# Kernel tuning notes

Hardware: AMD Instinct MI355X
Metric: run time of the kernel (lower is better)

The kernel has to match this reference:

```python
import jax, jax.numpy as jnp
from jax import lax
import numpy as np

KSIZE = 3        # patch-matching kernel
RATE = 2         # dilation/upsample rate
FUSE_K = 3       # fusion kernel size
SCALE = 10.0     # softmax scale
EPS = 1e-4


def _same_pads(size, k, s):
    # TF 'SAME' padding: total pad so out = ceil(size / s)
    out = -(-size // s)
    total = max(0, (out - 1) * s + k - size)
    top = total // 2
    return (top, total - top)


def _extract_patches(x, k, s):
    # x: [N,C,H,W] -> [N, L, C, k, k], SAME padding, row-major patch order
    ph = _same_pads(x.shape[2], k, s)
    pw = _same_pads(x.shape[3], k, s)
    p = lax.conv_general_dilated_patches(x, (k, k), (s, s), (ph, pw))
    N, _, Ho, Wo = p.shape
    C = x.shape[1]
    p = p.reshape(N, C, k, k, Ho * Wo)  # channel-major patch layout (matches torch unfold)
    return jnp.transpose(p, (0, 4, 1, 2, 3))


def setup_inputs() -> dict:
    key = jax.random.key(0)
    k1, k2 = jax.random.split(key)
    f = jax.random.normal(k1, (8, 96, 64, 64), dtype=jnp.float32)
    b = jax.random.normal(k2, (8, 96, 64, 64), dtype=jnp.float32)
    return {"f": f, "b": b}


def reference(f, b):
    # TF-style nearest-neighbor downsample (stride sampling)
    fs = f[:, :, ::RATE, ::RATE]
    bs = b[:, :, ::RATE, ::RATE]
    N, C, H, W = fs.shape  # downsampled dims; f and b share shape here
    L = H * W
    kernel = 2 * RATE

    # raw background patches for aggregation: [N, L, C, 2r, 2r]
    raw_w = _extract_patches(b, kernel, RATE)
    # matching patches from downsampled background: [N, L, C, 3, 3]
    w = _extract_patches(bs, KSIZE, 1)

    fuse_w = jnp.eye(FUSE_K, dtype=f.dtype).reshape(1, 1, FUSE_K, FUSE_K)
    ct_pad = kernel - 1 - 1  # conv_transpose padding=1 -> conv pad k-1-p = 2

    def attend(xi, wi, rwi):
        # xi: [C,H,W]; wi: [L,C,3,3]; rwi: [L,C,2r,2r]
        norm = jnp.sqrt(jnp.sum(wi * wi, axis=(1, 2, 3), keepdims=True))
        wn = wi / jnp.maximum(norm, EPS)
        # cosine-similarity correlation: [L,H,W]
        yi = lax.conv_general_dilated(xi[None], wn, (1, 1), ((1, 1), (1, 1)))[0]
        # fusion: identity-kernel convs over the [L_b, L_f] score map, both orientations
        y2 = yi.reshape(1, 1, L, L)
        y2 = lax.conv_general_dilated(y2, fuse_w, (1, 1), ((1, 1), (1, 1)))
        y2 = jnp.transpose(y2.reshape(H, W, H, W), (1, 0, 3, 2)).reshape(1, 1, L, L)
        y2 = lax.conv_general_dilated(y2, fuse_w, (1, 1), ((1, 1), (1, 1)))
        yi = jnp.transpose(y2.reshape(W, H, W, H), (1, 0, 3, 2)).reshape(L, H, W)
        # softmax over background patches (mask mm == 1 since mask is None)
        yi = jax.nn.softmax(yi * SCALE, axis=0)
        # conv_transpose2d(yi, rwi, stride=RATE, padding=1) / 4
        wct = jnp.flip(jnp.swapaxes(rwi, 0, 1), axis=(2, 3))  # [C, L, 2r, 2r]
        out = lax.conv_general_dilated(
            yi[None], wct, (1, 1), ((ct_pad, ct_pad), (ct_pad, ct_pad)),
            lhs_dilation=(RATE, RATE))[0]
        return out / 4.0

    y = jax.vmap(attend)(fs, w, raw_w)  # [N, C, H*RATE, W*RATE]
    return y.reshape(f.shape)
```

## Files before the change

kernel.cpp:

```cpp
#include <hip/hip_runtime.h>
#include <math.h>

#define NB 8
#define NC 96
#define HF 64
#define HS 32
#define L 1024
#define MN 1536

#define G_OFF    0ull
#define F1T_OFF  (8ull * 1024 * 1024)
#define YB_B     (64ull * 1024 * 1024)
#define RWT_B    (80ull * 1024 * 1024)
#define N_OFF    (27262976ull)
#define FS_OFF   (27271168ull)
#define BS_OFF   (28057600ull)
#define Z_OFF    0ull

typedef __attribute__((ext_vector_type(8))) short short8;
typedef __attribute__((ext_vector_type(4))) float float4v;

__device__ inline unsigned short f2bf(float x) {
    union { float f; unsigned u; } v; v.f = x;
    unsigned r = v.u + 0x7fff + ((v.u >> 16) & 1);
    return (unsigned short)(r >> 16);
}

__global__ void kprep(const float* __restrict__ f, const float* __restrict__ b,
                      float* __restrict__ ws) {
    int n = blockIdx.x, c = blockIdx.y, z = blockIdx.z;
    int t = threadIdx.x;
    if (z == 0) {
        const float* src = f + ((size_t)n * NC + c) * (HF * HF);
        float* dst = ws + FS_OFF + ((size_t)n * NC + c) * 1024;
        #pragma unroll
        for (int e = 0; e < 4; ++e) {
            int pos = t + e * 256;
            int i = pos >> 5, j = pos & 31;
            dst[pos] = src[(2 * i) * HF + 2 * j];
        }
        return;
    }
    __shared__ float pl[64][65];
    const float* bp = b + ((size_t)n * NC + c) * (HF * HF);
    for (int e = 0; e < 16; ++e) {
        int idx = t + e * 256;
        pl[idx >> 6][idx & 63] = bp[idx];
    }
    __syncthreads();
    float* bs = ws + BS_OFF + ((size_t)n * NC + c) * 1024;
    #pragma unroll
    for (int e = 0; e < 4; ++e) {
        int pos = t + e * 256;
        int i = pos >> 5, j = pos & 31;
        bs[pos] = pl[2 * i][2 * j];
    }
    unsigned short* RWtF = (unsigned short*)((char*)ws + RWT_B) + (size_t)n * MN * L
                           + (size_t)c * 32 * 512;
    #pragma unroll
    for (int uv = 0; uv < 16; ++uv) {
        int u = uv >> 2, v = uv & 3;
        for (int e = 0; e < 4; ++e) {
            int k = t + e * 256;
            int ly = k & 31, lx = k >> 5;
            int r = 2 * ly - 1 + u, s = 2 * lx - 1 + v;
            float val = (r >= 0 && r < HF && s >= 0 && s < HF) ? pl[r][s] : 0.f;
            int kc = k >> 5, qd = (k >> 3) & 3, j = k & 7;
            RWtF[(size_t)kc * 512 + (qd * 16 + uv) * 8 + j] = f2bf(val);
        }
    }
}

__global__ void k0_norm(float* __restrict__ ws) {
    int n = blockIdx.x;
    int t = threadIdx.x;
    int i = t >> 5, j = t & 31;
    __shared__ float sq[1024];
    const float* bsp = ws + BS_OFF + (size_t)n * NC * 1024;
    float s = 0.f;
    for (int c = 0; c < NC; ++c) {
        float v = bsp[(size_t)c * 1024 + t];
        s += v * v;
    }
    sq[t] = s;
    __syncthreads();
    float nsq = 0.f;
    #pragma unroll
    for (int dy = -1; dy <= 1; ++dy)
        #pragma unroll
        for (int dx = -1; dx <= 1; ++dx) {
            int ii = i + dy, jj = j + dx;
            if (ii >= 0 && ii < HS && jj >= 0 && jj < HS) nsq += sq[ii * HS + jj];
        }
    ws[N_OFF + (size_t)n * L + t] = 1.f / fmaxf(sqrtf(nsq), 1e-4f);
}

__global__ __launch_bounds__(256) void k1_gram(float* __restrict__ ws) {
    int n = blockIdx.x;
    int p0 = blockIdx.y * 128, l0 = blockIdx.z * 128;
    int t = threadIdx.x;
    int tp = t >> 4, tm = t & 15;
    __shared__ float Bt[32][132];
    __shared__ float Ft[32][132];
    float acc[8][8] = {};
    const float* bsp = ws + BS_OFF + (size_t)n * NC * 1024;
    const float* fsp = ws + FS_OFF + (size_t)n * NC * 1024;
    for (int c0 = 0; c0 < NC; c0 += 32) {
        #pragma unroll
        for (int e = 0; e < 4; ++e) {
            int idx = t + e * 256;
            int cl = idx >> 5, vq = idx & 31;
            *(float4*)&Bt[cl][vq * 4] =
                *(const float4*)&bsp[(size_t)(c0 + cl) * 1024 + l0 + vq * 4];
            *(float4*)&Ft[cl][vq * 4] =
                *(const float4*)&fsp[(size_t)(c0 + cl) * 1024 + p0 + vq * 4];
        }
        __syncthreads();
        for (int cl = 0; cl < 32; ++cl) {
            float4 a0 = *(const float4*)&Bt[cl][tp * 8];
            float4 a1 = *(const float4*)&Bt[cl][tp * 8 + 4];
            float4 b0 = *(const float4*)&Ft[cl][tm * 8];
            float4 b1 = *(const float4*)&Ft[cl][tm * 8 + 4];
            float av[8] = {a0.x, a0.y, a0.z, a0.w, a1.x, a1.y, a1.z, a1.w};
            float bv[8] = {b0.x, b0.y, b0.z, b0.w, b1.x, b1.y, b1.z, b1.w};
            #pragma unroll
            for (int aa = 0; aa < 8; ++aa)
                #pragma unroll
                for (int bb = 0; bb < 8; ++bb)
                    acc[aa][bb] += av[aa] * bv[bb];
        }
        __syncthreads();
    }
    float* G = ws + G_OFF + (size_t)n * L * L;
    #pragma unroll
    for (int aa = 0; aa < 8; ++aa) {
        int l = l0 + tp * 8 + aa;
        *(float4*)&G[(size_t)l * L + p0 + tm * 8] =
            make_float4(acc[aa][0], acc[aa][1], acc[aa][2], acc[aa][3]);
        *(float4*)&G[(size_t)l * L + p0 + tm * 8 + 4] =
            make_float4(acc[aa][4], acc[aa][5], acc[aa][6], acc[aa][7]);
    }
}

__global__ __launch_bounds__(256) void k23_score_fuse1t(float* __restrict__ ws) {
    int bid = blockIdx.x;
    int n = bid & 7;
    int tile = bid >> 3;
    int i0 = (tile >> 5) * 32, j0 = (tile & 31) * 32;
    int t = threadIdx.x;
    __shared__ float U[36][37];
    __shared__ float sA[34][35];
    __shared__ float sinv[34];
    const float* G = ws + G_OFF + (size_t)n * L * L;
    const float* invn = ws + N_OFF + (size_t)n * L;
    if (t < 34) {
        int l = i0 - 1 + t;
        sinv[t] = ((unsigned)l < L) ? invn[l] : 0.f;
    }
    for (int e = 0; e < 6; ++e) {
        int idx = t + e * 256;
        if (idx < 1296) {
            int a = idx / 36, bq = idx - a * 36;
            int l = i0 - 2 + a, p = j0 - 2 + bq;
            float s = 0.f;
            #pragma unroll
            for (int dy = -1; dy <= 1; ++dy) {
                int ll = l + dy * 32, pp = p + dy * 32;
                if ((unsigned)ll < L && (unsigned)pp < L)
                    s += G[(size_t)ll * L + pp];
            }
            U[a][bq] = s;
        }
    }
    __syncthreads();
    for (int e = 0; e < 5; ++e) {
        int idx = t + e * 256;
        if (idx < 1156) {
            int ih = idx / 34, jh = idx - ih * 34;
            int l = i0 - 1 + ih, p = j0 - 1 + jh;
            float a = 0.f;
            if ((unsigned)l < L && (unsigned)p < L) {
                int lx = l & 31, px = p & 31;
                float s = 0.f;
                #pragma unroll
                for (int dx = -1; dx <= 1; ++dx) {
                    bool ok = (unsigned)(lx + dx) < HS && (unsigned)(px + dx) < HS;
                    float u = U[ih + 1 + dx][jh + 1 + dx];
                    s += ok ? u : 0.f;
                }
                a = sinv[ih] * s;
            }
            sA[ih][jh] = a;
        }
    }
    __syncthreads();
    float* F1T = ws + F1T_OFF + (size_t)n * L * L;
    #pragma unroll
    for (int e = 0; e < 4; ++e) {
        int idx = t + e * 256;
        int jl = idx >> 5, il = idx & 31;
        float v = sA[il][jl] + sA[il + 1][jl + 1] + sA[il + 2][jl + 2];
        F1T[(size_t)(j0 + jl) * L + i0 + il] = v;
    }
}

__global__ __launch_bounds__(256) void k4_fuse2_softmax(float* __restrict__ ws) {
    int n = blockIdx.x, px = blockIdx.y, py0 = blockIdx.z * 4;
    int t = threadIdx.x;
    __shared__ float trow[6][32][33];
    const float* F1T = ws + F1T_OFF + (size_t)n * L * L;
    int Jbase = px * HS + py0;
    #pragma unroll
    for (int e = 0; e < 6; ++e) {
        int idx = t + e * 256;
        int d = idx >> 8, q = idx & 255;
        int Jd = Jbase + d - 1;
        float4 v = make_float4(0.f, 0.f, 0.f, 0.f);
        if ((unsigned)Jd < L) {
            int rd = (Jd & 31) * HS + (Jd >> 5);
            v = *(const float4*)&F1T[(size_t)rd * L + 4 * q];
        }
        int col = q >> 3, r0 = (4 * q) & 31;
        trow[d][r0 + 0][col] = v.x;
        trow[d][r0 + 1][col] = v.y;
        trow[d][r0 + 2][col] = v.z;
        trow[d][r0 + 3][col] = v.w;
    }
    __syncthreads();
    int w = t >> 6, ln = t & 63;
    int py = py0 + w;
    int p = py * HS + px;
    float vals[16];
    float mymax = -1e30f;
    #pragma unroll
    for (int e = 0; e < 16; ++e) {
        int k = e * 64 + ln;
        float v = 0.f;
        #pragma unroll
        for (int d = 0; d < 3; ++d) {
            int kd = k + d - 1;
            if ((unsigned)kd < L) v += trow[w + d][kd >> 5][kd & 31];
        }
        v *= 10.0f;
        vals[e] = v;
        mymax = fmaxf(mymax, v);
    }
    #pragma unroll
    for (int off = 32; off > 0; off >>= 1)
        mymax = fmaxf(mymax, __shfl_xor(mymax, off));
    float mysum = 0.f;
    #pragma unroll
    for (int e = 0; e < 16; ++e) { vals[e] = __expf(vals[e] - mymax); mysum += vals[e]; }
    #pragma unroll
    for (int off = 32; off > 0; off >>= 1)
        mysum += __shfl_xor(mysum, off);
    float rinv = 1.f / mysum;
    unsigned short* YbF = (unsigned short*)((char*)ws + YB_B) + (size_t)n * L * L;
    int pt = p >> 4, fr = p & 15;
    #pragma unroll
    for (int e = 0; e < 16; ++e) {
        int k = e * 64 + ln;
        int kc = k >> 5, qd = (k >> 3) & 3, j = k & 7;
        YbF[((size_t)pt * 32 + kc) * 512 + (qd * 16 + fr) * 8 + j] = f2bf(vals[e] * rinv);
    }
}

__global__ __launch_bounds__(256) void k6_mfma_z(float* __restrict__ ws) {
    int n = blockIdx.x;
    int wv = threadIdx.x >> 6, lane = threadIdx.x & 63;
    int pt0 = blockIdx.z * 8 + (wv >> 1) * 4;
    int mt0 = blockIdx.y * 8 + (wv & 1) * 4;

    const unsigned short* YbF = (const unsigned short*)((const char*)ws + YB_B)
                                + (size_t)n * L * L + lane * 8;
    const unsigned short* RWtF = (const unsigned short*)((const char*)ws + RWT_B)
                                 + (size_t)n * MN * L + lane * 8;

    float4v acc[4][4] = {};
    short8 af[2][4], bf[2][4];
    #pragma unroll
    for (int a = 0; a < 4; ++a) {
        af[0][a] = *(const short8*)(YbF + ((size_t)(pt0 + a) * 32) * 512);
        bf[0][a] = *(const short8*)(RWtF + ((size_t)(mt0 + a) * 32) * 512);
    }
    for (int kc = 0; kc < 32; ++kc) {
        int cur = kc & 1, nxt = cur ^ 1;
        if (kc < 31) {
            #pragma unroll
            for (int a = 0; a < 4; ++a) {
                af[nxt][a] = *(const short8*)(YbF + ((size_t)(pt0 + a) * 32 + kc + 1) * 512);
                bf[nxt][a] = *(const short8*)(RWtF + ((size_t)(mt0 + a) * 32 + kc + 1) * 512);
            }
        }
        #pragma unroll
        for (int a = 0; a < 4; ++a)
            #pragma unroll
            for (int bq = 0; bq < 4; ++bq)
                acc[a][bq] = __builtin_amdgcn_mfma_f32_16x16x32_bf16(
                    af[cur][a], bf[cur][bq], acc[a][bq], 0, 0, 0);
    }

    int fr = lane & 15, qd = lane >> 4;
    float* Zp = ws + Z_OFF + (size_t)n * L * MN;
    #pragma unroll
    for (int a = 0; a < 4; ++a) {
        #pragma unroll
        for (int r = 0; r < 4; ++r) {
            int p = (pt0 + a) * 16 + qd * 4 + r;
            #pragma unroll
            for (int bq = 0; bq < 4; ++bq) {
                int m = (mt0 + bq) * 16 + fr;
                Zp[(size_t)p * MN + m] = acc[a][bq][r];
            }
        }
    }
}

__global__ __launch_bounds__(256) void k7_gather(const float* __restrict__ ws,
                                                 float* __restrict__ out) {
    int n = blockIdx.x, yq = blockIdx.y, c = blockIdx.z;
    int t = threadIdx.x;
    int y0 = yq * 4;
    int ibase = (y0 >> 1) - 1;
    __shared__ float zs[128][17];
    const float* Zp = ws + Z_OFF + (size_t)n * L * MN;
    #pragma unroll
    for (int e = 0; e < 2; ++e) {
        int idx = t + e * 256;
        int pl = idx >> 2, q = idx & 3;
        int il = pl >> 5, j = pl & 31;
        int i = ibase + il;
        float4 v = make_float4(0.f, 0.f, 0.f, 0.f);
        if (i >= 0 && i < HS)
            v = *(const float4*)&Zp[(size_t)(i * HS + j) * MN + c * 16 + q * 4];
        zs[pl][q * 4 + 0] = v.x;
        zs[pl][q * 4 + 1] = v.y;
        zs[pl][q * 4 + 2] = v.z;
        zs[pl][q * 4 + 3] = v.w;
    }
    __syncthreads();
    int y = y0 + (t >> 6), x = t & 63;
    int ih = (y + 1) >> 1, jh = (x + 1) >> 1;
    float s = 0.f;
    #pragma unroll
    for (int di = 0; di < 2; ++di) {
        int i = ih - di;
        if (i < 0 || i >= HS) continue;
        int u = y + 1 - 2 * i;
        int il = i - ibase;
        #pragma unroll
        for (int dj = 0; dj < 2; ++dj) {
            int j = jh - dj;
            if (j < 0 || j >= HS) continue;
            int v = x + 1 - 2 * j;
            s += zs[il * 32 + j][u * 4 + v];
        }
    }
    out[(((size_t)n * NC + c) * HF + y) * HF + x] = 0.25f * s;
}

extern "C" void kernel_launch(void* const* d_in, const int* in_sizes, int n_in,
                              void* d_out, int out_size, void* d_ws, size_t ws_size,
                              hipStream_t stream) {
    const float* f = (const float*)d_in[0];
    const float* b = (const float*)d_in[1];
    float* out = (float*)d_out;
    float* ws = (float*)d_ws;

    kprep<<<dim3(NB, NC, 2), 256, 0, stream>>>(f, b, ws);
    k0_norm<<<NB, 1024, 0, stream>>>(ws);
    k1_gram<<<dim3(NB, 8, 8), 256, 0, stream>>>(ws);
    k23_score_fuse1t<<<8192, 256, 0, stream>>>(ws);
    k4_fuse2_softmax<<<dim3(NB, 32, 8), 256, 0, stream>>>(ws);
    k6_mfma_z<<<dim3(NB, 12, 8), 256, 0, stream>>>(ws);
    k7_gather<<<dim3(NB, 16, 96), 256, 0, stream>>>(ws, out);
}
```

Baseline: 200.7 us.

## Vectorize RWt packing stores, retile MFMA Z GEMM, gather two channels per block

```diff
diff --git a/kernel.cpp b/kernel.cpp
--- a/kernel.cpp
+++ b/kernel.cpp
@@ -57,17 +57,23 @@
     }
     unsigned short* RWtF = (unsigned short*)((char*)ws + RWT_B) + (size_t)n * MN * L
                            + (size_t)c * 32 * 512;
-    #pragma unroll
-    for (int uv = 0; uv < 16; ++uv) {
-        int u = uv >> 2, v = uv & 3;
-        for (int e = 0; e < 4; ++e) {
-            int k = t + e * 256;
-            int ly = k & 31, lx = k >> 5;
-            int r = 2 * ly - 1 + u, s = 2 * lx - 1 + v;
-            float val = (r >= 0 && r < HF && s >= 0 && s < HF) ? pl[r][s] : 0.f;
-            int kc = k >> 5, qd = (k >> 3) & 3, j = k & 7;
-            RWtF[(size_t)kc * 512 + (qd * 16 + uv) * 8 + j] = f2bf(val);
-        }
+    int wv = t >> 6, ln = t & 63;
+    int qd = ln >> 4, uv = ln & 15;
+    int u = uv >> 2, v = uv & 3;
+    #pragma unroll
+    for (int it = 0; it < 8; ++it) {
+        int kc = it * 4 + wv;
+        short8 out8;
+        int s = 2 * kc - 1 + v;
+        bool sok = (s >= 0 && s < HF);
+        #pragma unroll
+        for (int j = 0; j < 8; ++j) {
+            int ly = qd * 8 + j;
+            int r = 2 * ly - 1 + u;
+            float val = (sok && r >= 0 && r < HF) ? pl[r][s] : 0.f;
+            out8[j] = (short)f2bf(val);
+        }
+        *(short8*)(RWtF + (size_t)kc * 512 + ln * 8) = out8;
     }
 }
 
@@ -269,33 +275,35 @@
     int n = blockIdx.x;
     int wv = threadIdx.x >> 6, lane = threadIdx.x & 63;
     int pt0 = blockIdx.z * 8 + (wv >> 1) * 4;
-    int mt0 = blockIdx.y * 8 + (wv & 1) * 4;
+    int mt0 = blockIdx.y * 6 + (wv & 1) * 3;
 
     const unsigned short* YbF = (const unsigned short*)((const char*)ws + YB_B)
                                 + (size_t)n * L * L + lane * 8;
     const unsigned short* RWtF = (const unsigned short*)((const char*)ws + RWT_B)
                                  + (size_t)n * MN * L + lane * 8;
 
-    float4v acc[4][4] = {};
-    short8 af[2][4], bf[2][4];
-    #pragma unroll
-    for (int a = 0; a < 4; ++a) {
+    float4v acc[4][3] = {};
+    short8 af[2][4], bf[2][3];
+    #pragma unroll
+    for (int a = 0; a < 4; ++a)
         af[0][a] = *(const short8*)(YbF + ((size_t)(pt0 + a) * 32) * 512);
-        bf[0][a] = *(const short8*)(RWtF + ((size_t)(mt0 + a) * 32) * 512);
-    }
+    #pragma unroll
+    for (int bq = 0; bq < 3; ++bq)
+        bf[0][bq] = *(const short8*)(RWtF + ((size_t)(mt0 + bq) * 32) * 512);
     for (int kc = 0; kc < 32; ++kc) {
         int cur = kc & 1, nxt = cur ^ 1;
         if (kc < 31) {
             #pragma unroll
-            for (int a = 0; a < 4; ++a) {
+            for (int a = 0; a < 4; ++a)
                 af[nxt][a] = *(const short8*)(YbF + ((size_t)(pt0 + a) * 32 + kc + 1) * 512);
-                bf[nxt][a] = *(const short8*)(RWtF + ((size_t)(mt0 + a) * 32 + kc + 1) * 512);
-            }
+            #pragma unroll
+            for (int bq = 0; bq < 3; ++bq)
+                bf[nxt][bq] = *(const short8*)(RWtF + ((size_t)(mt0 + bq) * 32 + kc + 1) * 512);
         }
         #pragma unroll
         for (int a = 0; a < 4; ++a)
             #pragma unroll
-            for (int bq = 0; bq < 4; ++bq)
+            for (int bq = 0; bq < 3; ++bq)
                 acc[a][bq] = __builtin_amdgcn_mfma_f32_16x16x32_bf16(
                     af[cur][a], bf[cur][bq], acc[a][bq], 0, 0, 0);
     }
@@ -308,7 +316,7 @@
         for (int r = 0; r < 4; ++r) {
             int p = (pt0 + a) * 16 + qd * 4 + r;
             #pragma unroll
-            for (int bq = 0; bq < 4; ++bq) {
+            for (int bq = 0; bq < 3; ++bq) {
                 int m = (mt0 + bq) * 16 + fr;
                 Zp[(size_t)p * MN + m] = acc[a][bq][r];
             }
@@ -318,21 +326,21 @@
 
 __global__ __launch_bounds__(256) void k7_gather(const float* __restrict__ ws,
                                                  float* __restrict__ out) {
-    int n = blockIdx.x, yq = blockIdx.y, c = blockIdx.z;
+    int n = blockIdx.x, yq = blockIdx.y, c0 = blockIdx.z * 2;
     int t = threadIdx.x;
     int y0 = yq * 4;
     int ibase = (y0 >> 1) - 1;
-    __shared__ float zs[128][17];
+    __shared__ float zs[128][33];
     const float* Zp = ws + Z_OFF + (size_t)n * L * MN;
     #pragma unroll
-    for (int e = 0; e < 2; ++e) {
-        int idx = t + e * 256;
-        int pl = idx >> 2, q = idx & 3;
+    for (int e = 0; e < 4; ++e) {
+        int idx = t + e * 256;
+        int pl = idx >> 3, q = idx & 7;
         int il = pl >> 5, j = pl & 31;
         int i = ibase + il;
         float4 v = make_float4(0.f, 0.f, 0.f, 0.f);
         if (i >= 0 && i < HS)
-            v = *(const float4*)&Zp[(size_t)(i * HS + j) * MN + c * 16 + q * 4];
+            v = *(const float4*)&Zp[(size_t)(i * HS + j) * MN + c0 * 16 + q * 4];
         zs[pl][q * 4 + 0] = v.x;
         zs[pl][q * 4 + 1] = v.y;
         zs[pl][q * 4 + 2] = v.z;
@@ -341,7 +349,7 @@
     __syncthreads();
     int y = y0 + (t >> 6), x = t & 63;
     int ih = (y + 1) >> 1, jh = (x + 1) >> 1;
-    float s = 0.f;
+    float s0 = 0.f, s1 = 0.f;
     #pragma unroll
     for (int di = 0; di < 2; ++di) {
         int i = ih - di;
@@ -353,10 +361,12 @@
             int j = jh - dj;
             if (j < 0 || j >= HS) continue;
             int v = x + 1 - 2 * j;
-            s += zs[il * 32 + j][u * 4 + v];
-        }
-    }
-    out[(((size_t)n * NC + c) * HF + y) * HF + x] = 0.25f * s;
+            s0 += zs[il * 32 + j][u * 4 + v];
+            s1 += zs[il * 32 + j][16 + u * 4 + v];
+        }
+    }
+    out[(((size_t)n * NC + c0) * HF + y) * HF + x] = 0.25f * s0;
+    out[(((size_t)n * NC + c0 + 1) * HF + y) * HF + x] = 0.25f * s1;
 }
 
 extern "C" void kernel_launch(void* const* d_in, const int* in_sizes, int n_in,
@@ -372,6 +382,6 @@
     k1_gram<<<dim3(NB, 8, 8), 256, 0, stream>>>(ws);
     k23_score_fuse1t<<<8192, 256, 0, stream>>>(ws);
     k4_fuse2_softmax<<<dim3(NB, 32, 8), 256, 0, stream>>>(ws);
-    k6_mfma_z<<<dim3(NB, 12, 8), 256, 0, stream>>>(ws);
-    k7_gather<<<dim3(NB, 16, 96), 256, 0, stream>>>(ws, out);
-}
+    k6_mfma_z<<<dim3(NB, 16, 8), 256, 0, stream>>>(ws);
+    k7_gather<<<dim3(NB, 16, 48), 256, 0, stream>>>(ws, out);
+}
```

Result: slower. 211.1 us (+5.2%).
